# Kernel tuning notes

Measured on AMD Instinct MI355X. Metric: run time of the kernel, lower is better.

Reference implementation:

```python
import jax, jax.numpy as jnp
import numpy as np

EPS_DIST = 1e-8
EPS_BN = 1e-5


def _bn_relu(x, g, b):
    # training-mode BatchNorm1d over (batch, spatial) per channel, then ReLU
    mean = jnp.mean(x, axis=(0, 2), keepdims=True)
    var = jnp.mean((x - mean) ** 2, axis=(0, 2), keepdims=True)
    xhat = (x - mean) * jax.lax.rsqrt(var + EPS_BN)
    return jax.nn.relu(xhat * g[None, :, None] + b[None, :, None])


def setup_inputs() -> dict:
    key = jax.random.key(0)
    ks = jax.random.split(key, 8)
    B, N, M, C1, C2 = 8, 16384, 4096, 64, 256
    return {
        "p1": jax.random.normal(ks[0], (B, N, 3), jnp.float32),
        "p2": jax.random.normal(ks[1], (B, M, 3), jnp.float32),
        "f1": jax.random.normal(ks[2], (B, C1, N), jnp.float32),
        "f2": jax.random.normal(ks[3], (B, C2, M), jnp.float32),
        "idx": jax.random.randint(ks[4], (B, N, 3), 0, M, jnp.int64),
        "W1": jax.random.normal(ks[5], (256, C1 + C2), jnp.float32) * 0.05,
        "g1": jnp.ones((256,), jnp.float32),
        "b1": jnp.zeros((256,), jnp.float32),
        "W2": jax.random.normal(ks[6], (256, 256), jnp.float32) * 0.05,
        "g2": jnp.ones((256,), jnp.float32),
        "b2": jnp.zeros((256,), jnp.float32),
    }


def reference(p1, p2, f1, f2, idx, W1, g1, b1, W2, g2, b2):
    B = p1.shape[0]
    b_ix = jnp.arange(B)[:, None, None]  # batch index for gathers
    # --- three_interpolation: inverse-squared-distance weighted 3-NN interp ---
    nbr_xyz = p2[b_ix, idx]                     # [B, N, 3, 3]
    d2 = jnp.sum((p1[:, :, None, :] - nbr_xyz) ** 2, axis=-1)  # [B, N, 3]
    recip = 1.0 / (d2 + EPS_DIST)
    weight = recip / jnp.sum(recip, axis=-1, keepdims=True)    # [B, N, 3]
    f2_nbr = jnp.swapaxes(f2, 1, 2)[b_ix, idx]  # [B, N, 3, C2]
    interp = jnp.einsum("bnkc,bnk->bcn", f2_nbr, weight)       # [B, C2, N]
    # --- concat + two 1x1 conv + BN + ReLU blocks ---
    x = jnp.concatenate((f1, interp), axis=1)   # [B, C1+C2, N]
    x = _bn_relu(jnp.einsum("oi,bin->bon", W1, x), g1, b1)
    x = _bn_relu(jnp.einsum("oi,bin->bon", W2, x), g2, b2)
    return x
```

## Files before the change

kernel.cpp:

```cpp
#include <hip/hip_runtime.h>
#include <hip/hip_bf16.h>

#define BB 8
#define NN 16384
#define MM 4096
#define C1 64
#define C2 256
#define K1 320
#define CO 256
#define MTOT (BB * NN)

#define STATS_OFF 0
#define FLAG_OFF  8192
#define W1B_OFF   16384
#define W2B_OFF   180224
#define F2T_OFF   327680
#define XT_OFF    (327680 + 16777216)
#define H2_OFF    (327680 + 16777216 + 83886080)


typedef short v8s __attribute__((ext_vector_type(8)));
typedef float v4f __attribute__((ext_vector_type(4)));

__device__ __forceinline__ float bf2f(unsigned short u) {
    unsigned v = ((unsigned)u) << 16;
    float f;
    __builtin_memcpy(&f, &v, 4);
    return f;
}
__device__ __forceinline__ unsigned short f2bf(float f) {
    unsigned u;
    __builtin_memcpy(&u, &f, 4);
    unsigned r = u + 0x7fffu + ((u >> 16) & 1u);
    return (unsigned short)(r >> 16);
}
__device__ __forceinline__ void gload16(const unsigned short* g, unsigned short* l) {
    __builtin_amdgcn_global_load_lds((const __attribute__((address_space(1))) unsigned int*)g,
                                     (__attribute__((address_space(3))) unsigned int*)l, 16, 0, 0);
}

__global__ void k_pre(const void* idx_raw, int* flag64, float* stats,
                      const float* __restrict__ W1, unsigned short* __restrict__ W1b,
                      const float* __restrict__ W2, unsigned short* __restrict__ W2b,
                      const float* __restrict__ f2, unsigned short* __restrict__ f2t,
                      const float* __restrict__ f1, unsigned short* __restrict__ xT) {
    __shared__ float tile[64][33];
    int blk = blockIdx.x;
    int t = threadIdx.x;
    if (blk < 320) {
        int e = blk * 256 + t;
        int row = e / K1, col = e - row * K1;
        W1b[row * K1 + (col ^ ((row & 7) << 3))] = f2bf(W1[e]);
    } else if (blk < 576) {
        int e = (blk - 320) * 256 + t;
        int row = e >> 8, col = e & 255;
        W2b[row * CO + (col ^ ((row & 7) << 3))] = f2bf(W2[e]);
    } else if (blk == 576) {
        for (int i = t; i < 8 * 256; i += 256) stats[i] = 0.f;
        if (t == 0) {
            const int* a = (const int*)idx_raw;
            int all0 = 1;
            for (int j = 1; j < 64; j += 2) all0 &= (a[j] == 0);
            *flag64 = all0;
        }
    } else if (blk < 577 + 4096) {
        int i = blk - 577;
        int m0 = (i & 127) * 32;
        int c0 = ((i >> 7) & 3) * 64;
        int b = i >> 9;
        int lm = t & 31, lc = t >> 5;
        const float* src = f2 + ((size_t)b * C2 + c0) * MM + m0;
#pragma unroll
        for (int j = 0; j < 8; ++j)
            tile[lc + 8 * j][lm] = src[(size_t)(lc + 8 * j) * MM + lm];
        __syncthreads();
        int m = t >> 3, c8 = (t & 7) * 8;
        unsigned short tmp[8];
#pragma unroll
        for (int k = 0; k < 8; ++k) tmp[k] = f2bf(tile[c8 + k][m]);
        uint4 v;
        v.x = (unsigned)tmp[0] | ((unsigned)tmp[1] << 16);
        v.y = (unsigned)tmp[2] | ((unsigned)tmp[3] << 16);
        v.z = (unsigned)tmp[4] | ((unsigned)tmp[5] << 16);
        v.w = (unsigned)tmp[6] | ((unsigned)tmp[7] << 16);
        *(uint4*)&f2t[((size_t)b * MM + m0 + m) * C2 + c0 + c8] = v;
    } else {
        int i = blk - 4673;
        int n0 = (i & 511) * 32;
        int b = i >> 9;
        int lm = t & 31, lc = t >> 5;
        const float* src = f1 + ((size_t)b * C1) * NN + n0;
#pragma unroll
        for (int j = 0; j < 8; ++j)
            tile[lc + 8 * j][lm] = src[(size_t)(lc + 8 * j) * NN + lm];
        __syncthreads();
        int m = t >> 3, c8 = (t & 7) * 8;
        unsigned short tmp[8];
#pragma unroll
        for (int k = 0; k < 8; ++k) tmp[k] = f2bf(tile[c8 + k][m]);
        uint4 v;
        v.x = (unsigned)tmp[0] | ((unsigned)tmp[1] << 16);
        v.y = (unsigned)tmp[2] | ((unsigned)tmp[3] << 16);
        v.z = (unsigned)tmp[4] | ((unsigned)tmp[5] << 16);
        v.w = (unsigned)tmp[6] | ((unsigned)tmp[7] << 16);
        *(uint4*)&xT[((size_t)b * NN + n0 + m) * K1 + (c8 ^ ((m & 7) * 8))] = v;
    }
}

__global__ void k_interp(const float* __restrict__ p1, const float* __restrict__ p2,
                         const void* __restrict__ idxv, const int* __restrict__ flag64,
                         const unsigned short* __restrict__ f2t,
                         unsigned short* __restrict__ xT) {
    int t = threadIdx.x;
    int p = t >> 5, lane = t & 31;
    size_t pt = (size_t)blockIdx.x * 8 + p;
    int b = (int)(pt >> 14);
    int m0, m1, m2;
    if (*flag64) {
        const long long* id = (const long long*)idxv;
        m0 = (int)id[pt * 3 + 0]; m1 = (int)id[pt * 3 + 1]; m2 = (int)id[pt * 3 + 2];
    } else {
        const int* id = (const int*)idxv;
        m0 = id[pt * 3 + 0]; m1 = id[pt * 3 + 1]; m2 = id[pt * 3 + 2];
    }
    float qx = p1[pt * 3 + 0], qy = p1[pt * 3 + 1], qz = p1[pt * 3 + 2];
    const float* pb = p2 + (size_t)b * MM * 3;
    float dx, dy, dz;
    dx = qx - pb[m0 * 3 + 0]; dy = qy - pb[m0 * 3 + 1]; dz = qz - pb[m0 * 3 + 2];
    float d0 = dx * dx + dy * dy + dz * dz;
    dx = qx - pb[m1 * 3 + 0]; dy = qy - pb[m1 * 3 + 1]; dz = qz - pb[m1 * 3 + 2];
    float d1 = dx * dx + dy * dy + dz * dz;
    dx = qx - pb[m2 * 3 + 0]; dy = qy - pb[m2 * 3 + 1]; dz = qz - pb[m2 * 3 + 2];
    float d2v = dx * dx + dy * dy + dz * dz;
    float r0 = 1.f / (d0 + 1e-8f), r1 = 1.f / (d1 + 1e-8f), r2 = 1.f / (d2v + 1e-8f);
    float inv = 1.f / (r0 + r1 + r2);
    float w0 = r0 * inv, w1 = r1 * inv, w2 = r2 * inv;

    const unsigned short* fb = f2t + (size_t)b * MM * C2;
    int c0 = lane * 8;
    uint4 va = *(const uint4*)(fb + (size_t)m0 * C2 + c0);
    uint4 vb = *(const uint4*)(fb + (size_t)m1 * C2 + c0);
    uint4 vc = *(const uint4*)(fb + (size_t)m2 * C2 + c0);

    float r[8];
    {
        const unsigned av[4] = {va.x, va.y, va.z, va.w};
        const unsigned bv[4] = {vb.x, vb.y, vb.z, vb.w};
        const unsigned cv[4] = {vc.x, vc.y, vc.z, vc.w};
#pragma unroll
        for (int q = 0; q < 4; ++q) {
            r[2 * q + 0] = w0 * bf2f((unsigned short)(av[q] & 0xffff))
                         + w1 * bf2f((unsigned short)(bv[q] & 0xffff))
                         + w2 * bf2f((unsigned short)(cv[q] & 0xffff));
            r[2 * q + 1] = w0 * bf2f((unsigned short)(av[q] >> 16))
                         + w1 * bf2f((unsigned short)(bv[q] >> 16))
                         + w2 * bf2f((unsigned short)(cv[q] >> 16));
        }
    }
    uint4 outv;
    outv.x = (unsigned)f2bf(r[0]) | ((unsigned)f2bf(r[1]) << 16);
    outv.y = (unsigned)f2bf(r[2]) | ((unsigned)f2bf(r[3]) << 16);
    outv.z = (unsigned)f2bf(r[4]) | ((unsigned)f2bf(r[5]) << 16);
    outv.w = (unsigned)f2bf(r[6]) | ((unsigned)f2bf(r[7]) << 16);
    *(uint4*)(xT + pt * K1 + ((C1 + c0) ^ (((int)pt & 7) * 8))) = outv;
}

#define TM 128
#define TN 128
#define TK 64
__launch_bounds__(256)
__global__ void k_gemm1(const unsigned short* __restrict__ xT,
                        const unsigned short* __restrict__ W1b,
                        unsigned short* __restrict__ h1,
                        float* __restrict__ sum1, float* __restrict__ ssq1) {
    __shared__ unsigned short smem[2][TM * TK + TN * TK];
    const int t = threadIdx.x;
    const int lane = t & 63, w = t >> 6;
    const int wm = w >> 1, wc = w & 1;
    const long rbase = (long)blockIdx.y * TM;
    const int cb = blockIdx.x * TN;

    v4f acc[4][4];
#pragma unroll
    for (int r = 0; r < 4; ++r)
#pragma unroll
        for (int c = 0; c < 4; ++c) acc[r][c] = (v4f)(0.f);

    const int srow = w * 32 + (lane >> 3);
    const int sch = (lane & 7) * 8;
    const unsigned short* Ag = xT + (rbase + srow) * K1 + sch;
    const unsigned short* Bg = W1b + (size_t)(cb + srow) * K1 + sch;

    const int ln = lane & 15, q = lane >> 4;
    const int xs = (ln & 7) * 8;

#pragma unroll
    for (int j = 0; j < 4; ++j) {
        gload16(Ag + (size_t)(j * 8) * K1, smem[0] + (w * 32 + j * 8) * TK);
        gload16(Bg + (size_t)(j * 8) * K1, smem[0] + TM * TK + (w * 32 + j * 8) * TK);
    }

    for (int k0 = 0; k0 < K1; k0 += TK) {
        const int p = (k0 >> 6) & 1;
        if (k0 + TK < K1) {
#pragma unroll
            for (int j = 0; j < 4; ++j) {
                gload16(Ag + (size_t)(j * 8) * K1 + k0 + TK, smem[p ^ 1] + (w * 32 + j * 8) * TK);
                gload16(Bg + (size_t)(j * 8) * K1 + k0 + TK, smem[p ^ 1] + TM * TK + (w * 32 + j * 8) * TK);
            }
            asm volatile("s_waitcnt vmcnt(8)" ::: "memory");
        } else {
            asm volatile("s_waitcnt vmcnt(0)" ::: "memory");
        }
        asm volatile("s_barrier" ::: "memory");
        __builtin_amdgcn_sched_barrier(0);
        const unsigned short* ApL = smem[p] + (wm * 64 + ln) * TK;
        const unsigned short* BpL = smem[p] + TM * TK + (wc * 64 + ln) * TK;
#pragma unroll
        for (int ks = 0; ks < 2; ++ks) {
            const int off = (q * 8 + ks * 32) ^ xs;
            v8s af[4], bg[4];
#pragma unroll
            for (int r = 0; r < 4; ++r) af[r] = *(const v8s*)(ApL + r * 16 * TK + off);
#pragma unroll
            for (int c = 0; c < 4; ++c) bg[c] = *(const v8s*)(BpL + c * 16 * TK + off);
#pragma unroll
            for (int r = 0; r < 4; ++r)
#pragma unroll
                for (int c = 0; c < 4; ++c)
                    acc[r][c] = __builtin_amdgcn_mfma_f32_16x16x32_bf16(af[r], bg[c], acc[r][c], 0, 0, 0);
        }
        __builtin_amdgcn_sched_barrier(0);
        if (k0 + TK < K1) asm volatile("s_barrier" ::: "memory");
    }
    __syncthreads();

    unsigned short* ep = (unsigned short*)smem;
#pragma unroll
    for (int c = 0; c < 4; ++c) {
        int col = wc * 64 + c * 16 + ln;
        int cc = col >> 3, ci = col & 7;
        float s = 0.f, sq = 0.f;
#pragma unroll
        for (int r = 0; r < 4; ++r)
#pragma unroll
            for (int i = 0; i < 4; ++i) {
                int row = wm * 64 + r * 16 + q * 4 + i;
                float v = acc[r][c][i];
                ep[row * 128 + 8 * (cc ^ (row & 15)) + ci] = f2bf(v);
                s += v; sq += v * v;
            }
        s += __shfl_xor(s, 16); sq += __shfl_xor(sq, 16);
        s += __shfl_xor(s, 32); sq += __shfl_xor(sq, 32);
        if (lane < 16) {
            atomicAdd(&sum1[cb + col], s);
            atomicAdd(&ssq1[cb + col], sq);
        }
    }
    __syncthreads();
    {
        int rr = t >> 4, cc2 = t & 15;
#pragma unroll
        for (int j = 0; j < 8; ++j) {
            int row = rr + 16 * j;
            uint4 v = *(const uint4*)&ep[row * 128 + 8 * (cc2 ^ (row & 15))];
            *(uint4*)&h1[(size_t)(rbase + row) * CO + cb + cc2 * 8] = v;
        }
    }
}

__launch_bounds__(256)
__global__ void k_gemm2(const unsigned short* __restrict__ h1,
                        const unsigned short* __restrict__ W2b,
                        const float* __restrict__ sum1, const float* __restrict__ ssq1,
                        const float* __restrict__ g1, const float* __restrict__ b1,
                        unsigned short* __restrict__ h2,
                        float* __restrict__ sum2, float* __restrict__ ssq2) {
    __shared__ unsigned short smem[2][TM * TK + TN * TK];
    __shared__ float sc1[CO], sh1[CO];
    const int t = threadIdx.x;
    const int lane = t & 63, w = t >> 6;
    const int wm = w >> 1, wc = w & 1;
    const long rbase = (long)blockIdx.y * TM;
    const int cb = blockIdx.x * TN;

    {
        const float invn = 1.f / (float)MTOT;
        float m = sum1[t] * invn;
        float v = ssq1[t] * invn - m * m;
        float s = g1[t] * rsqrtf(v + 1e-5f);
        sc1[t] = s;
        sh1[t] = b1[t] - m * s;
    }
    __syncthreads();

    v4f acc[4][4];
#pragma unroll
    for (int r = 0; r < 4; ++r)
#pragma unroll
        for (int c = 0; c < 4; ++c) acc[r][c] = (v4f)(0.f);

    const int srow = w * 32 + (lane >> 3);
    const int sch = (lane & 7) * 8;
    const unsigned short* Ag = h1 + (rbase + srow) * CO + sch;
    const unsigned short* Bg = W2b + (size_t)(cb + srow) * CO + sch;
    const int awz = srow * TK + (sch ^ ((srow & 7) * 8));

    const int ln = lane & 15, q = lane >> 4;
    const int xs = (ln & 7) * 8;

#define CONV_STORE(AV, KOFF, BASE)                                                     \
    do {                                                                               \
        float4 sca = *(const float4*)(sc1 + (KOFF) + sch);                             \
        float4 scb = *(const float4*)(sc1 + (KOFF) + sch + 4);                         \
        float4 sha = *(const float4*)(sh1 + (KOFF) + sch);                             \
        float4 shb = *(const float4*)(sh1 + (KOFF) + sch + 4);                         \
        _Pragma("unroll")                                                              \
        for (int j = 0; j < 4; ++j) {                                                  \
            uint4 av = (AV)[j];                                                        \
            float y0 = fmaxf(bf2f((unsigned short)(av.x & 0xffff)) * sca.x + sha.x, 0.f); \
            float y1 = fmaxf(bf2f((unsigned short)(av.x >> 16)) * sca.y + sha.y, 0.f); \
            float y2 = fmaxf(bf2f((unsigned short)(av.y & 0xffff)) * sca.z + sha.z, 0.f); \
            float y3 = fmaxf(bf2f((unsigned short)(av.y >> 16)) * sca.w + sha.w, 0.f); \
            float y4 = fmaxf(bf2f((unsigned short)(av.z & 0xffff)) * scb.x + shb.x, 0.f); \
            float y5 = fmaxf(bf2f((unsigned short)(av.z >> 16)) * scb.y + shb.y, 0.f); \
            float y6 = fmaxf(bf2f((unsigned short)(av.w & 0xffff)) * scb.z + shb.z, 0.f); \
            float y7 = fmaxf(bf2f((unsigned short)(av.w >> 16)) * scb.w + shb.w, 0.f); \
            uint4 ov;                                                                  \
            ov.x = (unsigned)f2bf(y0) | ((unsigned)f2bf(y1) << 16);                    \
            ov.y = (unsigned)f2bf(y2) | ((unsigned)f2bf(y3) << 16);                    \
            ov.z = (unsigned)f2bf(y4) | ((unsigned)f2bf(y5) << 16);                    \
            ov.w = (unsigned)f2bf(y6) | ((unsigned)f2bf(y7) << 16);                    \
            *(uint4*)((BASE) + awz + (j * 8) * TK) = ov;                               \
        }                                                                              \
    } while (0)

    uint4 avc[4], avn[4];
#pragma unroll
    for (int j = 0; j < 4; ++j)
        gload16(Bg + (size_t)(j * 8) * CO, smem[0] + TM * TK + (w * 32 + j * 8) * TK);
#pragma unroll
    for (int j = 0; j < 4; ++j) avc[j] = *(const uint4*)(Ag + (size_t)(j * 8) * CO);
#pragma unroll
    for (int j = 0; j < 4; ++j) avn[j] = *(const uint4*)(Ag + (size_t)(j * 8) * CO + TK);
    CONV_STORE(avc, 0, smem[0]);
    __syncthreads();

#pragma unroll
    for (int kk = 0; kk < 4; ++kk) {
        const int p = kk & 1;
        if (kk < 3) {
#pragma unroll
            for (int j = 0; j < 4; ++j)
                gload16(Bg + (size_t)(j * 8) * CO + (kk + 1) * TK,
                        smem[p ^ 1] + TM * TK + (w * 32 + j * 8) * TK);
            CONV_STORE(avn, (kk + 1) * TK, smem[p ^ 1]);
        }
        if (kk < 2) {
#pragma unroll
            for (int j = 0; j < 4; ++j)
                avn[j] = *(const uint4*)(Ag + (size_t)(j * 8) * CO + (kk + 2) * TK);
        }
        const unsigned short* ApL = smem[p] + (wm * 64 + ln) * TK;
        const unsigned short* BpL = smem[p] + TM * TK + (wc * 64 + ln) * TK;
#pragma unroll
        for (int ks = 0; ks < 2; ++ks) {
            const int off = (q * 8 + ks * 32) ^ xs;
            v8s af[4], bg4[4];
#pragma unroll
            for (int r = 0; r < 4; ++r) af[r] = *(const v8s*)(ApL + r * 16 * TK + off);
#pragma unroll
            for (int c = 0; c < 4; ++c) bg4[c] = *(const v8s*)(BpL + c * 16 * TK + off);
#pragma unroll
            for (int r = 0; r < 4; ++r)
#pragma unroll
                for (int c = 0; c < 4; ++c)
                    acc[r][c] = __builtin_amdgcn_mfma_f32_16x16x32_bf16(af[r], bg4[c], acc[r][c], 0, 0, 0);
        }
        __syncthreads();
    }
#undef CONV_STORE

    unsigned short* ep = (unsigned short*)smem;
    const int b = (int)(rbase >> 14);
    const int nb = (int)(rbase & (NN - 1));
#pragma unroll
    for (int c = 0; c < 4; ++c) {
        int ol = wc * 64 + c * 16 + ln;
        float s = 0.f, sq = 0.f;
#pragma unroll
        for (int r = 0; r < 4; ++r)
#pragma unroll
            for (int i = 0; i < 4; ++i) {
                int row = wm * 64 + r * 16 + q * 4 + i;
                int rc = row >> 3, ri = row & 7;
                float v = acc[r][c][i];
                ep[ol * 128 + 8 * (rc ^ (ol & 15)) + ri] = f2bf(v);
                s += v; sq += v * v;
            }
        s += __shfl_xor(s, 16); sq += __shfl_xor(sq, 16);
        s += __shfl_xor(s, 32); sq += __shfl_xor(sq, 32);
        if (lane < 16) {
            atomicAdd(&sum2[cb + ol], s);
            atomicAdd(&ssq2[cb + ol], sq);
        }
    }
    __syncthreads();
    {
        int oo = t >> 4, nc = t & 15;
#pragma unroll
        for (int j = 0; j < 8; ++j) {
            int ol = oo + 16 * j;
            uint4 v = *(const uint4*)&ep[ol * 128 + 8 * (nc ^ (ol & 15))];
            *(uint4*)&h2[(((size_t)(b * CO + cb + ol)) << 14) + nb + nc * 8] = v;
        }
    }
}

__global__ void k_apply(const unsigned short* __restrict__ h2,
                        const float* __restrict__ sum2, const float* __restrict__ ssq2,
                        const float* __restrict__ g2, const float* __restrict__ b2,
                        float* __restrict__ out) {
    __shared__ float ss[2];
    int o = (blockIdx.x >> 3) & 255;
    if (threadIdx.x == 0) {
        const float invn = 1.f / (float)MTOT;
        float m = sum2[o] * invn;
        float v = ssq2[o] * invn - m * m;
        float s = g2[o] * rsqrtf(v + 1e-5f);
        ss[0] = s;
        ss[1] = b2[o] - m * s;
    }
    __syncthreads();
    float s = ss[0], d = ss[1];
    size_t i = ((size_t)blockIdx.x * 256 + threadIdx.x) * 8;
    uint4 hv = *(const uint4*)(h2 + i);
    float4 v0, v1;
    v0.x = fmaxf(bf2f((unsigned short)(hv.x & 0xffff)) * s + d, 0.f);
    v0.y = fmaxf(bf2f((unsigned short)(hv.x >> 16)) * s + d, 0.f);
    v0.z = fmaxf(bf2f((unsigned short)(hv.y & 0xffff)) * s + d, 0.f);
    v0.w = fmaxf(bf2f((unsigned short)(hv.y >> 16)) * s + d, 0.f);
    v1.x = fmaxf(bf2f((unsigned short)(hv.z & 0xffff)) * s + d, 0.f);
    v1.y = fmaxf(bf2f((unsigned short)(hv.z >> 16)) * s + d, 0.f);
    v1.z = fmaxf(bf2f((unsigned short)(hv.w & 0xffff)) * s + d, 0.f);
    v1.w = fmaxf(bf2f((unsigned short)(hv.w >> 16)) * s + d, 0.f);
    *(float4*)&out[i] = v0;
    *(float4*)&out[i + 4] = v1;
}

extern "C" void kernel_launch(void* const* d_in, const int* in_sizes, int n_in,
                              void* d_out, int out_size, void* d_ws, size_t ws_size,
                              hipStream_t stream) {
    const float* p1 = (const float*)d_in[0];
    const float* p2 = (const float*)d_in[1];
    const float* f1 = (const float*)d_in[2];
    const float* f2 = (const float*)d_in[3];
    const void*  idx = d_in[4];
    const float* W1 = (const float*)d_in[5];
    const float* g1 = (const float*)d_in[6];
    const float* b1 = (const float*)d_in[7];
    const float* W2 = (const float*)d_in[8];
    const float* g2 = (const float*)d_in[9];
    const float* b2 = (const float*)d_in[10];
    float* out = (float*)d_out;

    char* ws = (char*)d_ws;
    float* stats = (float*)(ws + STATS_OFF);
    float* sum1 = stats + 0;     float* ssq1 = stats + 256;
    float* sum2 = stats + 1024;  float* ssq2 = stats + 1280;
    int* flag64 = (int*)(ws + FLAG_OFF);
    unsigned short* W1b = (unsigned short*)(ws + W1B_OFF);
    unsigned short* W2b = (unsigned short*)(ws + W2B_OFF);
    unsigned short* f2t = (unsigned short*)(ws + F2T_OFF);
    unsigned short* xT  = (unsigned short*)(ws + XT_OFF);
    unsigned short* h2  = (unsigned short*)(ws + H2_OFF);

    unsigned short* h1 = (unsigned short*)d_out;

    k_pre<<<577 + 4096 + 4096, 256, 0, stream>>>(idx, flag64, stats, W1, W1b, W2, W2b,
                                                 f2, f2t, f1, xT);
    k_interp<<<MTOT / 8, 256, 0, stream>>>(p1, p2, idx, flag64, f2t, xT);
    k_gemm1<<<dim3(CO / TN, MTOT / TM), 256, 0, stream>>>(xT, W1b, h1, sum1, ssq1);
    k_gemm2<<<dim3(CO / TN, MTOT / TM), 256, 0, stream>>>(h1, W2b, sum1, ssq1, g1, b1, h2, sum2, ssq2);
    k_apply<<<(int)((size_t)out_size / 2048), 256, 0, stream>>>(h2, sum2, ssq2, g2, b2, out);
}
```

Measured before the change: 400.0 us.

## Preload all A tiles and hand-schedule the second GEMM pipeline with explicit waitcnts

The second conv GEMM now loads all four K-slices of the h1 activation tile into registers up front instead of double-buffering two slices. The k-loop is unrolled by macro and uses explicit s_waitcnt vmcnt/lgkmcnt, raw s_barrier and sched_barrier in place of __syncthreads, so global loads can stay in flight across stages. BN-apply packing now uses v_cvt_pk_bf16_f32 inline asm instead of manual bf16 conversion and packing, and the initial barrier after computing the scale/shift is moved. The cost is more registers held for the A tiles, which may lower occupancy, and the hand-counted vmcnt values are fragile if the compiler's memory-op ordering changes.

```diff
diff --git a/kernel.cpp b/kernel.cpp
--- a/kernel.cpp
+++ b/kernel.cpp
@@ -292,7 +292,6 @@
         sc1[t] = s;
         sh1[t] = b1[t] - m * s;
     }
-    __syncthreads();
 
     v4f acc[4][4];
 #pragma unroll
@@ -327,59 +326,71 @@
             float y6 = fmaxf(bf2f((unsigned short)(av.w & 0xffff)) * scb.z + shb.z, 0.f); \
             float y7 = fmaxf(bf2f((unsigned short)(av.w >> 16)) * scb.w + shb.w, 0.f); \
             uint4 ov;                                                                  \
-            ov.x = (unsigned)f2bf(y0) | ((unsigned)f2bf(y1) << 16);                    \
-            ov.y = (unsigned)f2bf(y2) | ((unsigned)f2bf(y3) << 16);                    \
-            ov.z = (unsigned)f2bf(y4) | ((unsigned)f2bf(y5) << 16);                    \
-            ov.w = (unsigned)f2bf(y6) | ((unsigned)f2bf(y7) << 16);                    \
+            asm("v_cvt_pk_bf16_f32 %0, %1, %2" : "=v"(ov.x) : "v"(y0), "v"(y1));       \
+            asm("v_cvt_pk_bf16_f32 %0, %1, %2" : "=v"(ov.y) : "v"(y2), "v"(y3));       \
+            asm("v_cvt_pk_bf16_f32 %0, %1, %2" : "=v"(ov.z) : "v"(y4), "v"(y5));       \
+            asm("v_cvt_pk_bf16_f32 %0, %1, %2" : "=v"(ov.w) : "v"(y6), "v"(y7));       \
             *(uint4*)((BASE) + awz + (j * 8) * TK) = ov;                               \
         }                                                                              \
     } while (0)
 
-    uint4 avc[4], avn[4];
+    uint4 a[4][4];
 #pragma unroll
     for (int j = 0; j < 4; ++j)
         gload16(Bg + (size_t)(j * 8) * CO, smem[0] + TM * TK + (w * 32 + j * 8) * TK);
 #pragma unroll
-    for (int j = 0; j < 4; ++j) avc[j] = *(const uint4*)(Ag + (size_t)(j * 8) * CO);
-#pragma unroll
-    for (int j = 0; j < 4; ++j) avn[j] = *(const uint4*)(Ag + (size_t)(j * 8) * CO + TK);
-    CONV_STORE(avc, 0, smem[0]);
-    __syncthreads();
-
-#pragma unroll
-    for (int kk = 0; kk < 4; ++kk) {
-        const int p = kk & 1;
-        if (kk < 3) {
-#pragma unroll
-            for (int j = 0; j < 4; ++j)
-                gload16(Bg + (size_t)(j * 8) * CO + (kk + 1) * TK,
-                        smem[p ^ 1] + TM * TK + (w * 32 + j * 8) * TK);
-            CONV_STORE(avn, (kk + 1) * TK, smem[p ^ 1]);
-        }
-        if (kk < 2) {
-#pragma unroll
-            for (int j = 0; j < 4; ++j)
-                avn[j] = *(const uint4*)(Ag + (size_t)(j * 8) * CO + (kk + 2) * TK);
-        }
-        const unsigned short* ApL = smem[p] + (wm * 64 + ln) * TK;
-        const unsigned short* BpL = smem[p] + TM * TK + (wc * 64 + ln) * TK;
-#pragma unroll
-        for (int ks = 0; ks < 2; ++ks) {
-            const int off = (q * 8 + ks * 32) ^ xs;
-            v8s af[4], bg4[4];
-#pragma unroll
-            for (int r = 0; r < 4; ++r) af[r] = *(const v8s*)(ApL + r * 16 * TK + off);
-#pragma unroll
-            for (int c = 0; c < 4; ++c) bg4[c] = *(const v8s*)(BpL + c * 16 * TK + off);
-#pragma unroll
-            for (int r = 0; r < 4; ++r)
-#pragma unroll
-                for (int c = 0; c < 4; ++c)
-                    acc[r][c] = __builtin_amdgcn_mfma_f32_16x16x32_bf16(af[r], bg4[c], acc[r][c], 0, 0, 0);
-        }
-        __syncthreads();
-    }
+    for (int kk = 0; kk < 4; ++kk)
+#pragma unroll
+        for (int j = 0; j < 4; ++j)
+            a[kk][j] = *(const uint4*)(Ag + (size_t)(j * 8) * CO + kk * TK);
+    __syncthreads();
+    CONV_STORE(a[0], 0, smem[0]);
+    __syncthreads();
+
+#define G2_ITER(KK, P)                                                                 \
+    do {                                                                               \
+        if ((KK) < 3) {                                                                \
+            _Pragma("unroll")                                                          \
+            for (int j = 0; j < 4; ++j)                                                \
+                gload16(Bg + (size_t)(j * 8) * CO + ((KK) + 1) * TK,                   \
+                        smem[(P) ^ 1] + TM * TK + (w * 32 + j * 8) * TK);              \
+            CONV_STORE(a[(KK) + 1], ((KK) + 1) * TK, smem[(P) ^ 1]);                   \
+            asm volatile("s_waitcnt vmcnt(4)" ::: "memory");                           \
+        } else {                                                                       \
+            asm volatile("s_waitcnt vmcnt(0)" ::: "memory");                           \
+        }                                                                              \
+        asm volatile("s_barrier" ::: "memory");                                        \
+        __builtin_amdgcn_sched_barrier(0);                                             \
+        {                                                                              \
+            const unsigned short* ApL = smem[P] + (wm * 64 + ln) * TK;                 \
+            const unsigned short* BpL = smem[P] + TM * TK + (wc * 64 + ln) * TK;       \
+            _Pragma("unroll")                                                          \
+            for (int ks = 0; ks < 2; ++ks) {                                           \
+                const int off = (q * 8 + ks * 32) ^ xs;                                \
+                v8s af[4], bg4[4];                                                     \
+                _Pragma("unroll")                                                      \
+                for (int r = 0; r < 4; ++r) af[r] = *(const v8s*)(ApL + r * 16 * TK + off); \
+                _Pragma("unroll")                                                      \
+                for (int c = 0; c < 4; ++c) bg4[c] = *(const v8s*)(BpL + c * 16 * TK + off); \
+                _Pragma("unroll")                                                      \
+                for (int r = 0; r < 4; ++r)                                            \
+                    _Pragma("unroll")                                                  \
+                    for (int c = 0; c < 4; ++c)                                        \
+                        acc[r][c] = __builtin_amdgcn_mfma_f32_16x16x32_bf16(af[r], bg4[c], acc[r][c], 0, 0, 0); \
+            }                                                                          \
+        }                                                                              \
+        __builtin_amdgcn_sched_barrier(0);                                             \
+        asm volatile("s_waitcnt lgkmcnt(0)" ::: "memory");                             \
+        if ((KK) < 3) asm volatile("s_barrier" ::: "memory");                          \
+    } while (0)
+
+    G2_ITER(0, 0);
+    G2_ITER(1, 1);
+    G2_ITER(2, 0);
+    G2_ITER(3, 1);
+#undef G2_ITER
 #undef CONV_STORE
+    __syncthreads();
 
     unsigned short* ep = (unsigned short*)smem;
     const int b = (int)(rbase >> 14);
```

After: 408.5 us. +2.1%, slower.
